# Performance work log

Hardware: AMD Instinct MI355X
Metric: run time of the kernel (lower is better)

The kernel has to match this reference:

```python
import jax, jax.numpy as jnp
import numpy as np

NUM_ORDERS = 100
NUM_MACHINES = 40
NUM_AGVS = 64
EMBED = 128


def setup_inputs() -> dict:
    key = jax.random.key(0)
    ks = jax.random.split(key, 12)
    s = 0.05
    h_order = jax.random.normal(ks[0], (NUM_ORDERS, EMBED), jnp.float32)
    h_agv = jax.random.normal(ks[1], (NUM_AGVS, EMBED), jnp.float32)
    h_waiting = jax.random.normal(ks[2], (NUM_MACHINES, EMBED), jnp.float32)
    h_buffer = jax.random.normal(ks[3], (NUM_MACHINES, EMBED), jnp.float32)
    W1d = jax.random.normal(ks[4], (3 * EMBED, EMBED), jnp.float32) * s
    b1d = jnp.zeros((EMBED,), jnp.float32)
    W2d = jax.random.normal(ks[5], (EMBED,), jnp.float32) * s
    b2d = jnp.zeros((1,), jnp.float32)
    W1p = jax.random.normal(ks[6], (2 * EMBED, EMBED), jnp.float32) * s
    b1p = jnp.zeros((EMBED,), jnp.float32)
    W2p = jax.random.normal(ks[7], (EMBED,), jnp.float32) * s
    b2p = jnp.zeros((1,), jnp.float32)
    n_logits = NUM_AGVS * (NUM_ORDERS * NUM_MACHINES + NUM_MACHINES)
    action_mask = jax.random.randint(ks[8], (n_logits,), 0, 2).astype(jnp.int32)
    return dict(h_order=h_order, h_agv=h_agv, h_waiting=h_waiting, h_buffer=h_buffer,
                W1d=W1d, b1d=b1d, W2d=W2d, b2d=b2d,
                W1p=W1p, b1p=b1p, W2p=W2p, b2p=b2p,
                action_mask=action_mask)


def reference(h_order, h_agv, h_waiting, h_buffer,
              W1d, b1d, W2d, b2d, W1p, b1p, W2p, b2p, action_mask):
    O, M, A, D = NUM_ORDERS, NUM_MACHINES, NUM_AGVS, EMBED
    # dispatch pairs: order_idx = repeat_interleave(arange(O), M); machine_idx = tile(arange(M), O)
    order_idx = jnp.repeat(jnp.arange(O), M)            # [O*M]
    machine_idx = jnp.tile(jnp.arange(M), O)            # [O*M]
    pair = jnp.concatenate([h_order[order_idx], h_waiting[machine_idx]], axis=1)  # [O*M, 2D]
    agv_b = jnp.broadcast_to(h_agv[:, None, :], (A, O * M, D))                    # [A, O*M, D]
    disp_in = jnp.concatenate([agv_b, jnp.broadcast_to(pair[None], (A, O * M, 2 * D))], axis=-1)  # [A, O*M, 3D]
    hdd = jax.nn.relu(jnp.einsum('apf,fh->aph', disp_in, W1d) + b1d)
    disp_scores = jnp.einsum('aph,h->ap', hdd, W2d) + b2d[0]                      # [A, O*M]
    # pickup: concat(agv, buffer) per machine
    agv_p = jnp.broadcast_to(h_agv[:, None, :], (A, M, D))
    pick_in = jnp.concatenate([agv_p, jnp.broadcast_to(h_buffer[None], (A, M, D))], axis=-1)  # [A, M, 2D]
    hpp = jax.nn.relu(jnp.einsum('amf,fh->amh', pick_in, W1p) + b1p)
    pick_scores = jnp.einsum('amh,h->am', hpp, W2p) + b2p[0]                      # [A, M]
    logits = jnp.concatenate([disp_scores, pick_scores], axis=1).reshape(-1)      # [A*(O*M+M)]
    logits = jnp.where(action_mask == 0, -jnp.inf, logits)
    return logits
```

## Files before the change

kernel.cpp:

```cpp
#include <hip/hip_runtime.h>
#include <hip/hip_fp16.h>

#define NO 100
#define NM 40
#define NA 64
#define ND 128
#define PITCH 132

#define MASK_SENTINEL_BITS 0xFBFFu

typedef __half f16_t;
__device__ __forceinline__ float h2f(f16_t h) { return __half2float(h); }


__global__ __launch_bounds__(512) void proj_kernel(
    const f16_t* __restrict__ h_order,
    const f16_t* __restrict__ h_agv,
    const f16_t* __restrict__ h_waiting,
    const f16_t* __restrict__ h_buffer,
    const f16_t* __restrict__ W1d,
    const f16_t* __restrict__ b1d,
    const f16_t* __restrict__ W1p,
    const f16_t* __restrict__ b1p,
    float* __restrict__ ws) {
  const int row = blockIdx.x;
  const int tid = threadIdx.x;
  const int col = tid & 127;
  const int q = tid >> 7;

  const f16_t* in;
  const f16_t* W;
  const f16_t* bias = nullptr;
  float* out;

  if (row < NA) {
    in = h_agv + row * ND;            W = W1d;                bias = b1d;
    out = ws + row * ND;
  } else if (row < NA + NO) {
    int r = row - NA;
    in = h_order + r * ND;            W = W1d + ND * ND;
    out = ws + (NA + r) * ND;
  } else if (row < NA + NO + NM) {
    int r = row - NA - NO;
    in = h_waiting + r * ND;          W = W1d + 2 * ND * ND;
    out = ws + (NA + NO + r) * ND;
  } else if (row < NA + NO + NM + NA) {
    int r = row - NA - NO - NM;
    in = h_agv + r * ND;              W = W1p;                bias = b1p;
    out = ws + (NA + NO + NM + r) * ND;
  } else {
    int r = row - NA - NO - NM - NA;
    in = h_buffer + r * ND;           W = W1p + ND * ND;
    out = ws + (NA + NO + NM + NA + r) * ND;
  }

  __shared__ float sIn[ND];
  __shared__ float sPart[4 * ND];
  if (tid < ND) sIn[tid] = h2f(in[tid]);
  __syncthreads();

  float acc = 0.0f;
  const f16_t* Wq = W + (q * 32) * ND + col;
#pragma unroll 8
  for (int f = 0; f < 32; ++f) {
    acc += sIn[q * 32 + f] * h2f(Wq[f * ND]);
  }
  sPart[q * ND + col] = acc;
  __syncthreads();
  if (tid < ND) {
    float r = sPart[tid] + sPart[ND + tid] + sPart[2 * ND + tid] +
              sPart[3 * ND + tid] + (bias ? h2f(bias[tid]) : 0.0f);
    out[tid] = r;
  }
}

__global__ __launch_bounds__(256) void score_kernel(
    const float* __restrict__ ws,
    const f16_t* __restrict__ W2d,
    const f16_t* __restrict__ b2d,
    const f16_t* __restrict__ W2p,
    const f16_t* __restrict__ b2p,
    const int* __restrict__ mask,
    unsigned short* __restrict__ out) {
  __shared__ float lds[48 * PITCH + ND];
  const int tid = threadIdx.x;
  const int bid = blockIdx.x;
  const int per_agv = NO * NM + NM;

  if (bid < 512) {
    const int a = bid >> 3;
    const int o0 = ((bid & 7) >> 1) * 25;
    const int m0 = (bid & 1) * 20;
    float* spo = lds;
    float* spw = lds + 25 * PITCH;
    float* sw2 = lds + 45 * PITCH;

    const float4* paRow = (const float4*)(ws + a * ND);
    const float4* poBase = (const float4*)(ws + (NA + o0) * ND);
    for (int idx = tid; idx < 25 * (ND / 4); idx += 256) {
      int o = idx >> 5, c = idx & 31;
      float4 va = paRow[c], vo = poBase[o * (ND / 4) + c];
      *(float4*)(spo + o * PITCH + 4 * c) =
          make_float4(va.x + vo.x, va.y + vo.y, va.z + vo.z, va.w + vo.w);
    }
    const float4* pwBase = (const float4*)(ws + (NA + NO + m0) * ND);
    for (int idx = tid; idx < 20 * (ND / 4); idx += 256) {
      int m = idx >> 5, c = idx & 31;
      *(float4*)(spw + m * PITCH + 4 * c) = pwBase[m * (ND / 4) + c];
    }
    if (tid < ND) sw2[tid] = h2f(W2d[tid]);
    __syncthreads();

    if (tid >= 250) return;
    const int o = tid / 10;
    const int mb = tid % 10;
    const float* po_ = spo + o * PITCH;
    const float* pw_ = spw + mb * PITCH;

    float acc0 = 0.f, acc1 = 0.f;
#pragma unroll 8
    for (int i = 0; i < ND / 4; ++i) {
      float4 vo = *(const float4*)(po_ + 4 * i);
      float4 w0 = *(const float4*)(pw_ + 4 * i);
      float4 w1 = *(const float4*)(pw_ + 10 * PITCH + 4 * i);
      float4 ww = *(const float4*)(sw2 + 4 * i);
      acc0 += fmaxf(vo.x + w0.x, 0.f) * ww.x + fmaxf(vo.y + w0.y, 0.f) * ww.y +
              fmaxf(vo.z + w0.z, 0.f) * ww.z + fmaxf(vo.w + w0.w, 0.f) * ww.w;
      acc1 += fmaxf(vo.x + w1.x, 0.f) * ww.x + fmaxf(vo.y + w1.y, 0.f) * ww.y +
              fmaxf(vo.z + w1.z, 0.f) * ww.z + fmaxf(vo.w + w1.w, 0.f) * ww.w;
    }
    const float bd = h2f(b2d[0]);
    const int nbase = a * per_agv + (o0 + o) * NM + m0 + mb;
    float accs[2] = {acc0, acc1};
#pragma unroll
    for (int j = 0; j < 2; ++j) {
      int n = nbase + 10 * j;
      float val = fminf(fmaxf(accs[j] + bd, -60000.0f), 60000.0f);
      __half hv = __float2half(val);
      out[n] = (mask[n] == 0) ? (unsigned short)MASK_SENTINEL_BITS
                              : *(unsigned short*)&hv;
    }
  } else {
    const int a0 = (bid - 512) * 8;
    float* spa = lds;
    float* spb = lds + 8 * PITCH;
    float* sw2 = lds + 48 * PITCH;

    const float4* paBase = (const float4*)(ws + (NA + NO + NM) * ND);
    const float4* pbBase = (const float4*)(ws + (NA + NO + NM + NA) * ND);
    for (int idx = tid; idx < 8 * (ND / 4); idx += 256) {
      int r = idx >> 5, c = idx & 31;
      *(float4*)(spa + r * PITCH + 4 * c) = paBase[(a0 + r) * (ND / 4) + c];
    }
    for (int idx = tid; idx < 40 * (ND / 4); idx += 256) {
      int m = idx >> 5, c = idx & 31;
      *(float4*)(spb + m * PITCH + 4 * c) = pbBase[m * (ND / 4) + c];
    }
    if (tid < ND) sw2[tid] = h2f(W2p[tid]);
    __syncthreads();

    const float bp = h2f(b2p[0]);
    for (int p = tid; p < 8 * NM; p += 256) {
      const int a = a0 + p / NM;
      const int m = p % NM;
      const float* pa_ = spa + (p / NM) * PITCH;
      const float* pb_ = spb + m * PITCH;
      float acc = 0.f;
#pragma unroll 8
      for (int i = 0; i < ND / 4; ++i) {
        float4 va = *(const float4*)(pa_ + 4 * i);
        float4 vb = *(const float4*)(pb_ + 4 * i);
        float4 ww = *(const float4*)(sw2 + 4 * i);
        acc += fmaxf(va.x + vb.x, 0.f) * ww.x + fmaxf(va.y + vb.y, 0.f) * ww.y +
               fmaxf(va.z + vb.z, 0.f) * ww.z + fmaxf(va.w + vb.w, 0.f) * ww.w;
      }
      float val = fminf(fmaxf(acc + bp, -60000.0f), 60000.0f);
      int n = a * per_agv + NO * NM + m;
      __half hv = __float2half(val);
      out[n] = (mask[n] == 0) ? (unsigned short)MASK_SENTINEL_BITS
                              : *(unsigned short*)&hv;
    }
  }
}

extern "C" void kernel_launch(void* const* d_in, const int* in_sizes, int n_in,
                              void* d_out, int out_size, void* d_ws, size_t ws_size,
                              hipStream_t stream) {
  const f16_t* h_order   = (const f16_t*)d_in[0];
  const f16_t* h_agv     = (const f16_t*)d_in[1];
  const f16_t* h_waiting = (const f16_t*)d_in[2];
  const f16_t* h_buffer  = (const f16_t*)d_in[3];
  const f16_t* W1d       = (const f16_t*)d_in[4];
  const f16_t* b1d       = (const f16_t*)d_in[5];
  const f16_t* W2d       = (const f16_t*)d_in[6];
  const f16_t* b2d       = (const f16_t*)d_in[7];
  const f16_t* W1p       = (const f16_t*)d_in[8];
  const f16_t* b1p       = (const f16_t*)d_in[9];
  const f16_t* W2p       = (const f16_t*)d_in[10];
  const f16_t* b2p       = (const f16_t*)d_in[11];
  const int*   mask      = (const int*)d_in[12];
  unsigned short* out = (unsigned short*)d_out;
  float* ws = (float*)d_ws;

  proj_kernel<<<308, 512, 0, stream>>>(h_order, h_agv, h_waiting, h_buffer,
                                       W1d, b1d, W1p, b1p, ws);

  score_kernel<<<520, 256, 0, stream>>>(ws, W2d, b2d, W2p, b2p, mask, out);
}
```

Before: 89.57 us.

## Fuse projection and scoring kernels with per-row global flag synchronization

Merges the projection and score kernels into a single launch. The first 308 blocks compute projection rows and then publish per-row magic flags in workspace memory. Score blocks spin on the flags for the rows they need before loading them. This removes the second launch and the gap between kernels. It relies on all 520 blocks being co-resident, and the flags are never reset, so stale flags from an earlier call could let a block read rows that are not yet written. It also halves the projection block to 256 threads, with each thread loading half2 weight pairs.

```diff
diff --git a/kernel.cpp b/kernel.cpp
--- a/kernel.cpp
+++ b/kernel.cpp
@@ -9,11 +9,17 @@
 
 #define MASK_SENTINEL_BITS 0xFBFFu
 
+#define NROWS 308
+#define FLAG1_OFF 39424
+#define FLAG2_OFF 39936
+#define MAGIC1 0x6D1A4F2Bu
+#define MAGIC2 0x38C7E95Du
+
 typedef __half f16_t;
 __device__ __forceinline__ float h2f(f16_t h) { return __half2float(h); }
 
 
-__global__ __launch_bounds__(512) void proj_kernel(
+__global__ __launch_bounds__(256, 3) void fused_kernel(
     const f16_t* __restrict__ h_order,
     const f16_t* __restrict__ h_agv,
     const f16_t* __restrict__ h_waiting,
@@ -22,75 +28,92 @@
     const f16_t* __restrict__ b1d,
     const f16_t* __restrict__ W1p,
     const f16_t* __restrict__ b1p,
-    float* __restrict__ ws) {
-  const int row = blockIdx.x;
-  const int tid = threadIdx.x;
-  const int col = tid & 127;
-  const int q = tid >> 7;
-
-  const f16_t* in;
-  const f16_t* W;
-  const f16_t* bias = nullptr;
-  float* out;
-
-  if (row < NA) {
-    in = h_agv + row * ND;            W = W1d;                bias = b1d;
-    out = ws + row * ND;
-  } else if (row < NA + NO) {
-    int r = row - NA;
-    in = h_order + r * ND;            W = W1d + ND * ND;
-    out = ws + (NA + r) * ND;
-  } else if (row < NA + NO + NM) {
-    int r = row - NA - NO;
-    in = h_waiting + r * ND;          W = W1d + 2 * ND * ND;
-    out = ws + (NA + NO + r) * ND;
-  } else if (row < NA + NO + NM + NA) {
-    int r = row - NA - NO - NM;
-    in = h_agv + r * ND;              W = W1p;                bias = b1p;
-    out = ws + (NA + NO + NM + r) * ND;
-  } else {
-    int r = row - NA - NO - NM - NA;
-    in = h_buffer + r * ND;           W = W1p + ND * ND;
-    out = ws + (NA + NO + NM + NA + r) * ND;
-  }
-
-  __shared__ float sIn[ND];
-  __shared__ float sPart[4 * ND];
-  if (tid < ND) sIn[tid] = h2f(in[tid]);
-  __syncthreads();
-
-  float acc = 0.0f;
-  const f16_t* Wq = W + (q * 32) * ND + col;
-#pragma unroll 8
-  for (int f = 0; f < 32; ++f) {
-    acc += sIn[q * 32 + f] * h2f(Wq[f * ND]);
-  }
-  sPart[q * ND + col] = acc;
-  __syncthreads();
-  if (tid < ND) {
-    float r = sPart[tid] + sPart[ND + tid] + sPart[2 * ND + tid] +
-              sPart[3 * ND + tid] + (bias ? h2f(bias[tid]) : 0.0f);
-    out[tid] = r;
-  }
-}
-
-__global__ __launch_bounds__(256) void score_kernel(
-    const float* __restrict__ ws,
     const f16_t* __restrict__ W2d,
     const f16_t* __restrict__ b2d,
     const f16_t* __restrict__ W2p,
     const f16_t* __restrict__ b2p,
     const int* __restrict__ mask,
-    unsigned short* __restrict__ out) {
-  __shared__ float lds[48 * PITCH + ND];
+    unsigned short* __restrict__ out,
+    float* __restrict__ ws) {
   const int tid = threadIdx.x;
   const int bid = blockIdx.x;
   const int per_agv = NO * NM + NM;
+  __shared__ float lds[48 * PITCH + ND];
+  unsigned int* flags1 = reinterpret_cast<unsigned int*>(ws) + FLAG1_OFF;
+  unsigned int* flags2 = reinterpret_cast<unsigned int*>(ws) + FLAG2_OFF;
+
+  if (bid < NROWS) {
+    const int row = bid;
+    const f16_t* in;
+    const f16_t* W;
+    const f16_t* bias = nullptr;
+    float* prow = ws + row * ND;
+
+    if (row < NA) {
+      in = h_agv + row * ND;                  W = W1d;            bias = b1d;
+    } else if (row < NA + NO) {
+      in = h_order + (row - NA) * ND;         W = W1d + ND * ND;
+    } else if (row < NA + NO + NM) {
+      in = h_waiting + (row - NA - NO) * ND;  W = W1d + 2 * ND * ND;
+    } else if (row < NA + NO + NM + NA) {
+      in = h_agv + (row - NA - NO - NM) * ND; W = W1p;            bias = b1p;
+    } else {
+      in = h_buffer + (row - NA - NO - NM - NA) * ND; W = W1p + ND * ND;
+    }
+
+    float* sIn = lds;
+    float* sPart = lds + ND;
+    if (tid < ND) sIn[tid] = h2f(in[tid]);
+    __syncthreads();
+
+    const int c0 = (tid & 63) * 2;
+    const int q = tid >> 6;
+    float a0 = 0.0f, a1 = 0.0f;
+    const f16_t* Wq = W + (q * 32) * ND + c0;
+#pragma unroll 8
+    for (int f = 0; f < 32; ++f) {
+      __half2 w2 = *(const __half2*)(Wq + f * ND);
+      float s = sIn[q * 32 + f];
+      a0 += s * __low2float(w2);
+      a1 += s * __high2float(w2);
+    }
+    sPart[q * ND + c0] = a0;
+    sPart[q * ND + c0 + 1] = a1;
+    __syncthreads();
+    if (tid < ND) {
+      float r = sPart[tid] + sPart[ND + tid] + sPart[2 * ND + tid] +
+                sPart[3 * ND + tid] + (bias ? h2f(bias[tid]) : 0.0f);
+      prow[tid] = r;
+    }
+    __syncthreads();
+    if (tid == 0) {
+      __threadfence();
+      __hip_atomic_store(&flags1[row], MAGIC1 + (unsigned)row,
+                         __ATOMIC_RELAXED, __HIP_MEMORY_SCOPE_AGENT);
+      __hip_atomic_store(&flags2[row], MAGIC2 + (unsigned)row,
+                         __ATOMIC_RELAXED, __HIP_MEMORY_SCOPE_AGENT);
+    }
+  }
 
   if (bid < 512) {
     const int a = bid >> 3;
     const int o0 = ((bid & 7) >> 1) * 25;
     const int m0 = (bid & 1) * 20;
+
+    if (tid < 46) {
+      int row = (tid == 0) ? a
+              : (tid <= 25) ? (NA + o0 + (tid - 1))
+                            : (NA + NO + m0 + (tid - 26));
+      while (__hip_atomic_load(&flags1[row], __ATOMIC_RELAXED,
+                               __HIP_MEMORY_SCOPE_AGENT) !=
+             MAGIC1 + (unsigned)row) {}
+      while (__hip_atomic_load(&flags2[row], __ATOMIC_RELAXED,
+                               __HIP_MEMORY_SCOPE_AGENT) !=
+             MAGIC2 + (unsigned)row) {}
+    }
+    __syncthreads();
+    __threadfence();
+
     float* spo = lds;
     float* spw = lds + 25 * PITCH;
     float* sw2 = lds + 45 * PITCH;
@@ -142,6 +165,20 @@
     }
   } else {
     const int a0 = (bid - 512) * 8;
+
+    if (tid < 48) {
+      int row = (tid < 8) ? (NA + NO + NM + a0 + tid)
+                          : (NA + NO + NM + NA + (tid - 8));
+      while (__hip_atomic_load(&flags1[row], __ATOMIC_RELAXED,
+                               __HIP_MEMORY_SCOPE_AGENT) !=
+             MAGIC1 + (unsigned)row) {}
+      while (__hip_atomic_load(&flags2[row], __ATOMIC_RELAXED,
+                               __HIP_MEMORY_SCOPE_AGENT) !=
+             MAGIC2 + (unsigned)row) {}
+    }
+    __syncthreads();
+    __threadfence();
+
     float* spa = lds;
     float* spb = lds + 8 * PITCH;
     float* sw2 = lds + 48 * PITCH;
@@ -202,8 +239,8 @@
   unsigned short* out = (unsigned short*)d_out;
   float* ws = (float*)d_ws;
 
-  proj_kernel<<<308, 512, 0, stream>>>(h_order, h_agv, h_waiting, h_buffer,
-                                       W1d, b1d, W1p, b1p, ws);
-
-  score_kernel<<<520, 256, 0, stream>>>(ws, W2d, b2d, W2p, b2p, mask, out);
+  fused_kernel<<<520, 256, 0, stream>>>(h_order, h_agv, h_waiting, h_buffer,
+                                        W1d, b1d, W1p, b1p,
+                                        W2d, b2d, W2p, b2p,
+                                        mask, out, ws);
 }
```

Result: slower. 126.4 us (+41.1%).
